# Optimization experiments

Hardware: AMD Instinct MI355X
Metric: run time of the kernel (lower is better)

The kernel has to match this reference:

```python
import jax, jax.numpy as jnp
import numpy as np

H = 8          # heads
KP = 6         # num_sparse keypoint tokens per group
NUM_PATCHES = 256


def _build_mask(N, Nk):
    # mask_q: [H, 3, N] bool, query token (g=0, i=0) disabled
    mask_q = np.ones((H, 3, N), dtype=bool)
    mask_q[:, 0, 0] = False
    # mask_k: [H, 3, Nk] bool, key token j=0 disabled for all groups
    mask_k = np.ones((H, 3, Nk), dtype=bool)
    mask_k[:, :, 0] = False
    keep = mask_q[:, :, :, None] & mask_k[:, :, None, :]  # [H,3,N,Nk]
    return jnp.asarray(~keep)  # True where masked out


def setup_inputs() -> dict:
    key = jax.random.key(0)
    k1, k2, k3 = jax.random.split(key, 3)
    B, G, N, D = 64, 3, NUM_PATCHES + KP, 512
    x = jax.random.normal(k1, (B, G, N, D), dtype=jnp.float32)
    w_qkv = jax.random.normal(k2, (D, 3 * D), dtype=jnp.float32) * (D ** -0.5)
    w_out = jax.random.normal(k3, (D, D), dtype=jnp.float32) * (D ** -0.5)
    b_out = jnp.zeros((D,), dtype=jnp.float32)
    return {"x": x, "w_qkv": w_qkv, "w_out": w_out, "b_out": b_out}


def reference(x, w_qkv, w_out, b_out):
    B, G, N, D = x.shape
    Dh = D // H
    scale = D ** -0.5  # scale_with_head=False

    qkv = x @ w_qkv  # [B,G,N,3D]
    q, k, v = jnp.split(qkv, 3, axis=-1)

    def to_heads(t):  # b g n (h d) -> b h g n d
        return t.reshape(B, G, N, H, Dh).transpose(0, 3, 1, 2, 4)

    q, k, v = to_heads(q), to_heads(k), to_heads(v)

    # gather keypoint K/V from all groups, shared across every group
    k_kp = k[:, :, :, :KP].reshape(B, H, 1, G * KP, Dh)
    v_kp = v[:, :, :, :KP].reshape(B, H, 1, G * KP, Dh)
    k_kp = jnp.broadcast_to(k_kp, (B, H, G, G * KP, Dh))
    v_kp = jnp.broadcast_to(v_kp, (B, H, G, G * KP, Dh))
    k = jnp.concatenate([k_kp, k[:, :, :, KP:]], axis=3)  # [B,H,G,Nk,Dh]
    v = jnp.concatenate([v_kp, v[:, :, :, KP:]], axis=3)
    Nk = k.shape[3]

    dots = jnp.einsum('bhgid,bhgjd->bhgij', q, k) * scale
    masked = _build_mask(N, Nk)  # [H,3,N,Nk], broadcasts over B
    neg = -jnp.finfo(dots.dtype).max
    dots = jnp.where(masked[None], neg, dots)

    attn = jax.nn.softmax(dots, axis=-1)
    out = jnp.einsum('bhgij,bhgjd->bhgid', attn, v)
    out = out.transpose(0, 2, 3, 1, 4).reshape(B, G, N, D)  # b h g n d -> b g n (h d)
    out = out @ w_out + b_out
    return out, dots
```

## Files before the change

kernel.cpp:

```cpp
#include <hip/hip_runtime.h>
#include <float.h>
#include <math.h>

#define B_   64
#define G_   3
#define N_   262
#define D_   512
#define H_   8
#define DH   64
#define KP_  6
#define NKP  18
#define NK   274
#define TD3  1536
#define M_   50304
#define SCALE 0.044194173824159216f
#define LOG2E 1.4426950408889634f

typedef unsigned short u16;
typedef __attribute__((ext_vector_type(4))) float f32x4;
typedef __attribute__((ext_vector_type(2))) float f32x2;
typedef float f32x4u __attribute__((ext_vector_type(4), aligned(4)));
typedef __attribute__((ext_vector_type(4))) unsigned int u32x4;
typedef __attribute__((ext_vector_type(8))) short bf16x8;

__device__ __forceinline__ u16 f2bf(float f) {
    unsigned int u = __float_as_uint(f);
    u += 0x7FFFu + ((u >> 16) & 1u);
    return (u16)(u >> 16);
}
__device__ __forceinline__ unsigned pack2bf(float lo, float hi) {
    unsigned ul = __float_as_uint(lo); ul += 0x7FFFu + ((ul >> 16) & 1u);
    unsigned uh = __float_as_uint(hi); uh += 0x7FFFu + ((uh >> 16) & 1u);
    return (ul >> 16) | (uh & 0xFFFF0000u);
}
__device__ __forceinline__ float mask_val() { return __uint_as_float(0xFF7F0000u); }

__device__ __forceinline__ void gload16(const void* g, void* l) {
    __builtin_amdgcn_global_load_lds(
        (const __attribute__((address_space(1))) unsigned int*)g,
        (__attribute__((address_space(3))) unsigned int*)l, 16, 0, 0);
}

__device__ __forceinline__ int xcd_swz(int orig, int nwg) {
    int q = nwg >> 3, r = nwg & 7;
    int xcd = orig & 7, lin = orig >> 3;
    return (xcd < r ? xcd * (q + 1) : r * (q + 1) + (xcd - r) * q) + lin;
}

__global__ __launch_bounds__(256)
void tcast2(const float* __restrict__ w1, u16* __restrict__ wT1,
            const float* __restrict__ w2, u16* __restrict__ wT2)
{
    int idx = blockIdx.x * 256 + threadIdx.x;
    if (idx < TD3 * D_) {
        int nn = idx / D_, kk = idx - nn * D_;
        wT1[idx] = f2bf(w1[(size_t)kk * TD3 + nn]);
    } else {
        int j = idx - TD3 * D_;
        if (j < D_ * D_) {
            int nn = j / D_, kk = j - nn * D_;
            wT2[j] = f2bf(w2[(size_t)kk * D_ + nn]);
        }
    }
}

template<int AF32, int OUT_BF16>
__global__ __launch_bounds__(512)
void gemm_bf16(const float* __restrict__ Af, const u16* __restrict__ Ab,
               const u16* __restrict__ WT,
               float* __restrict__ Cf, u16* __restrict__ Cb,
               const float* __restrict__ bias, int Ndim, int Kdim)
{
    __shared__ u16 Asm[128 * 64];
    __shared__ u16 Bsm[256 * 64];

    const int tid  = threadIdx.x;
    const int lane = tid & 63;
    const int wid  = tid >> 6;
    const int l15  = lane & 15;
    const int lg   = lane >> 4;
    const int wr   = (wid & 1) * 64;
    const int wc   = (wid >> 1) * 64;

    const int GX   = Ndim / 256;
    const int v    = xcd_swz(blockIdx.x, gridDim.x);
    const int row0 = (v / GX) * 128;
    const int col0 = (v % GX) * 256;

    const float* fsrcA[2];
    const u16*   bsrcA[2];
    #pragma unroll
    for (int i = 0; i < 2; ++i) {
        int slot = i * 512 + tid;
        int r = slot >> 3;
        int sblk = (slot & 7) ^ (r & 7);
        if (AF32) fsrcA[i] = Af + (size_t)(row0 + r) * Kdim + sblk * 8;
        else      bsrcA[i] = Ab + (size_t)(row0 + r) * Kdim + sblk * 8;
    }
    const u16* srcB[4];
    #pragma unroll
    for (int i = 0; i < 4; ++i) {
        int slot = i * 512 + tid;
        int r = slot >> 3;
        int sblk = (slot & 7) ^ (r & 7);
        srcB[i] = WT + (size_t)(col0 + r) * Kdim + sblk * 8;
    }

    f32x4 acc[4][4] = {};

    for (int k0 = 0; k0 < Kdim; k0 += 64) {
        #pragma unroll
        for (int i = 0; i < 4; ++i)
            gload16(srcB[i] + k0, &Bsm[(i * 512 + wid * 64) * 8]);
        if (AF32) {
            #pragma unroll
            for (int i = 0; i < 2; ++i) {
                float4 v0 = *(const float4*)(fsrcA[i] + k0);
                float4 v1 = *(const float4*)(fsrcA[i] + k0 + 4);
                u16 t[8] = { f2bf(v0.x), f2bf(v0.y), f2bf(v0.z), f2bf(v0.w),
                             f2bf(v1.x), f2bf(v1.y), f2bf(v1.z), f2bf(v1.w) };
                *(uint4*)&Asm[(i * 512 + tid) * 8] = *(const uint4*)t;
            }
        } else {
            #pragma unroll
            for (int i = 0; i < 2; ++i)
                gload16(bsrcA[i] + k0, &Asm[(i * 512 + wid * 64) * 8]);
        }
        __syncthreads();
        #pragma unroll
        for (int kk = 0; kk < 2; ++kk) {
            const int xb = (kk * 4 + lg) ^ (l15 & 7);
            bf16x8 a[4], b[4];
            #pragma unroll
            for (int m = 0; m < 4; ++m) a[m] = *(const bf16x8*)&Asm[(wr + m * 16 + l15) * 64 + xb * 8];
            #pragma unroll
            for (int n = 0; n < 4; ++n) b[n] = *(const bf16x8*)&Bsm[(wc + n * 16 + l15) * 64 + xb * 8];
            #pragma unroll
            for (int m = 0; m < 4; ++m)
                #pragma unroll
                for (int n = 0; n < 4; ++n)
                    acc[m][n] = __builtin_amdgcn_mfma_f32_16x16x32_bf16(a[m], b[n], acc[m][n], 0, 0, 0);
        }
        __syncthreads();
    }

    if (OUT_BF16) {
        u16* ob = (wid < 4) ? &Asm[wid * 2048] : &Bsm[(wid - 4) * 2048];
        #pragma unroll
        for (int p = 0; p < 2; ++p) {
            #pragma unroll
            for (int mh = 0; mh < 2; ++mh) {
                const int m = 2 * p + mh;
                #pragma unroll
                for (int n = 0; n < 4; ++n)
                    #pragma unroll
                    for (int r = 0; r < 4; ++r)
                        ob[(mh * 16 + lg * 4 + r) * 64 + n * 16 + l15] = f2bf(acc[m][n][r]);
            }
            #pragma unroll
            for (int it = 0; it < 4; ++it) {
                const int ch = it * 64 + lane;
                const int rw = ch >> 3, cp = ch & 7;
                u32x4 vv = *(const u32x4*)&ob[rw * 64 + cp * 8];
                *(u32x4*)(Cb + (size_t)(row0 + wr + p * 32 + rw) * Ndim + col0 + wc + cp * 8) = vv;
            }
        }
        return;
    }

    const int rbase = row0 + wr + lg * 4;
    const int cbase = col0 + wc + l15;
    #pragma unroll
    for (int m = 0; m < 4; ++m)
        #pragma unroll
        for (int n = 0; n < 4; ++n) {
            const int col = cbase + n * 16;
            #pragma unroll
            for (int r = 0; r < 4; ++r) {
                const int row = rbase + m * 16 + r;
                Cf[(size_t)row * Ndim + col] = acc[m][n][r] + bias[col];
            }
        }
}

__global__ __launch_bounds__(768, 1)
void attn_bf16(const u16* __restrict__ qkv, float* __restrict__ dots,
               u16* __restrict__ otmp)
{
    __shared__ u16 Ks[288 * 72];
    __shared__ u16 Vt[64 * 296];
    __shared__ float rowbuf[12][4 * 276];

    const int tid  = threadIdx.x;
    const int lane = tid & 63;
    const int wid  = tid >> 6;
    const int l15  = lane & 15;
    const int lg   = lane >> 4;

    const int bhg = blockIdx.x;
    const int b   = bhg / (H_ * G_);
    const int h   = (bhg / G_) % H_;
    const int g   = bhg % G_;
    const int rowbase = (b * G_ + g) * N_;
    const size_t dbase0 = (((size_t)(b * H_ + h) * G_ + g) * N_) * NK;

    #pragma unroll
    for (int it = 0; it < 3; ++it) {
        int lin = tid + it * 768;
        {
            int tok = lin >> 3, kg = (lin & 7) << 3;
            uint4 kv = make_uint4(0, 0, 0, 0), vv = make_uint4(0, 0, 0, 0);
            if (tok < NK) {
                int gs, ns;
                if (tok < NKP) { gs = tok / KP_; ns = tok - gs * KP_; }
                else           { gs = g;         ns = tok - NKP + KP_; }
                const u16* p = qkv + ((size_t)((b * G_ + gs) * N_ + ns)) * TD3 + h * DH + kg;
                kv = *(const uint4*)(p + D_);
                vv = *(const uint4*)(p + 2 * D_);
            }
            *(uint4*)&Ks[tok * 72 + kg] = kv;
            int slot = ((tok >> 5) << 5) | (((tok & 15) >> 2) << 3) | (((tok >> 4) & 1) << 2) | (tok & 3);
            union { uint4 u4; u16 us[8]; } u; u.u4 = vv;
            #pragma unroll
            for (int e = 0; e < 8; ++e) Vt[(kg + e) * 296 + slot] = u.us[e];
        }
    }
    __syncthreads();

    float* rb = rowbuf[wid];

    for (int t = wid; t < 17; t += 12) {
        const int n0 = t * 16;
        int qrow = n0 + l15; if (qrow > N_ - 1) qrow = N_ - 1;
        const u16* qp = qkv + (size_t)(rowbase + qrow) * TD3 + h * DH;
        bf16x8 qa0 = *(const bf16x8*)(qp + lg * 8);
        bf16x8 qa1 = *(const bf16x8*)(qp + 32 + lg * 8);

        f32x4 c[18];
        __builtin_amdgcn_s_setprio(1);
        #pragma unroll
        for (int jt = 0; jt < 18; ++jt) {
            const u16* kr = &Ks[(jt * 16 + l15) * 72];
            bf16x8 kb0 = *(const bf16x8*)(kr + lg * 8);
            bf16x8 kb1 = *(const bf16x8*)(kr + 32 + lg * 8);
            f32x4 z = {};
            z = __builtin_amdgcn_mfma_f32_16x16x32_bf16(kb0, qa0, z, 0, 0, 0);
            c[jt] = __builtin_amdgcn_mfma_f32_16x16x32_bf16(kb1, qa1, z, 0, 0, 0);
        }
        __builtin_amdgcn_s_setprio(0);

        #pragma unroll
        for (int jt = 0; jt < 18; ++jt)
            #pragma unroll
            for (int rr = 0; rr < 4; ++rr) c[jt][rr] *= SCALE;
        c[0][0] = (lg == 0) ? mask_val() : c[0][0];
        if (g == 0 && t == 0) {
            #pragma unroll
            for (int jt = 0; jt < 18; ++jt)
                #pragma unroll
                for (int rr = 0; rr < 4; ++rr)
                    c[jt][rr] = (l15 == 0) ? mask_val() : c[jt][rr];
        }

        const int php = l15 >> 2;
        const int r4  = l15 & 3;
        #pragma unroll
        for (int ph = 0; ph < 4; ++ph) {
            if (php == ph) {
                float* rr_ = &rb[r4 * 276];
                #pragma unroll
                for (int jt = 0; jt < 17; ++jt)
                    *(f32x4*)&rr_[jt * 16 + 4 * lg] = c[jt];
                if (lg == 0) { f32x2 tl = { c[17][0], c[17][1] }; *(f32x2*)&rr_[272] = tl; }
            }
            const int base_row = n0 + 4 * ph;
            #pragma unroll
            for (int r = 0; r < 4; ++r) {
                const int row = base_row + r;
                if (row < N_) {
                    const float* rrb = &rb[r * 276];
                    float* gp = &dots[dbase0 + (size_t)row * NK];
                    #pragma unroll
                    for (int i2 = 0; i2 < 2; ++i2) {
                        int ch = lane + (i2 << 6);
                        if (ch < 68) {
                            f32x4u vv = *(const f32x4*)&rrb[ch * 4];
                            __builtin_nontemporal_store(vv, (f32x4u*)&gp[ch * 4]);
                        } else if (ch == 68) {
                            f32x2 v2 = *(const f32x2*)&rrb[272];
                            __builtin_nontemporal_store(v2, (f32x2*)&gp[272]);
                        }
                    }
                }
            }
        }

        c[17][2] = -INFINITY; c[17][3] = -INFINITY;
        c[17][0] = (lg == 0) ? c[17][0] : -INFINITY;
        c[17][1] = (lg == 0) ? c[17][1] : -INFINITY;

        float mx = c[0][0];
        #pragma unroll
        for (int jt = 0; jt < 18; ++jt)
            #pragma unroll
            for (int rr = 0; rr < 4; ++rr) mx = fmaxf(mx, c[jt][rr]);
        mx = fmaxf(mx, __shfl_xor(mx, 16, 64));
        mx = fmaxf(mx, __shfl_xor(mx, 32, 64));
        float s = 0.f;
        #pragma unroll
        for (int jt = 0; jt < 18; ++jt)
            #pragma unroll
            for (int rr = 0; rr < 4; ++rr) {
                float p = exp2f((c[jt][rr] - mx) * LOG2E);
                c[jt][rr] = p;
                s += p;
            }
        s += __shfl_xor(s, 16, 64);
        s += __shfl_xor(s, 32, 64);
        const float inv = 1.f / s;

        f32x4 o[4] = {};
        __builtin_amdgcn_s_setprio(1);
        #pragma unroll
        for (int sl = 0; sl < 9; ++sl) {
            union { bf16x8 v; unsigned u[4]; } pa;
            pa.u[0] = pack2bf(c[2 * sl][0],     c[2 * sl][1]);
            pa.u[1] = pack2bf(c[2 * sl][2],     c[2 * sl][3]);
            pa.u[2] = pack2bf(c[2 * sl + 1][0], c[2 * sl + 1][1]);
            pa.u[3] = pack2bf(c[2 * sl + 1][2], c[2 * sl + 1][3]);
            #pragma unroll
            for (int dt = 0; dt < 4; ++dt) {
                bf16x8 vb = *(const bf16x8*)&Vt[(dt * 16 + l15) * 296 + sl * 32 + lg * 8];
                o[dt] = __builtin_amdgcn_mfma_f32_16x16x32_bf16(pa.v, vb, o[dt], 0, 0, 0);
            }
        }
        __builtin_amdgcn_s_setprio(0);

        u16* ob = (u16*)rb;
        #pragma unroll
        for (int dt = 0; dt < 4; ++dt)
            #pragma unroll
            for (int rr = 0; rr < 4; ++rr) {
                const int q = lg * 4 + rr;
                const float iq = __shfl(inv, q, 64);
                ob[q * 64 + dt * 16 + l15] = f2bf(o[dt][rr] * iq);
            }
        {
            const int vrows = min(16, N_ - n0);
            const int nch = vrows * 8;
            #pragma unroll
            for (int i2 = 0; i2 < 2; ++i2) {
                int ch = lane + (i2 << 6);
                if (ch < nch) {
                    int r = ch >> 3, cp = ch & 7;
                    uint4 vv = *(const uint4*)&ob[ch * 8];
                    *(uint4*)(otmp + (size_t)(rowbase + n0 + r) * D_ + h * DH + cp * 8) = vv;
                }
            }
        }
    }
}

extern "C" void kernel_launch(void* const* d_in, const int* in_sizes, int n_in,
                              void* d_out, int out_size, void* d_ws, size_t ws_size,
                              hipStream_t stream)
{
    const float* x     = (const float*)d_in[0];
    const float* w_qkv = (const float*)d_in[1];
    const float* w_out = (const float*)d_in[2];
    const float* b_out = (const float*)d_in[3];

    float* out  = (float*)d_out;
    float* dots = out + (size_t)M_ * D_;

    u16* wqkvT = (u16*)d_ws;
    u16* woutT = wqkvT + (size_t)TD3 * D_;
    u16* qkvb  = woutT + (size_t)D_ * D_;
    u16* otmpb = qkvb  + (size_t)M_ * TD3;

    tcast2<<<(TD3 * D_ + D_ * D_ + 255) / 256, 256, 0, stream>>>(
        w_qkv, wqkvT, w_out, woutT);

    gemm_bf16<1, 1><<<(TD3 / 256) * (M_ / 128), 512, 0, stream>>>(
        x, nullptr, wqkvT, nullptr, qkvb, nullptr, TD3, D_);

    attn_bf16<<<dim3(B_ * H_ * G_), 768, 0, stream>>>(qkvb, dots, otmpb);

    gemm_bf16<0, 0><<<(D_ / 256) * (M_ / 128), 512, 0, stream>>>(
        nullptr, otmpb, woutT, out, nullptr, b_out, D_, D_);
}
```

Measured before the change: 341.6 us.

## Double-buffer GEMM LDS tiles with BK=32 and prefetch next K-tile

```diff
diff --git a/kernel.cpp b/kernel.cpp
--- a/kernel.cpp
+++ b/kernel.cpp
@@ -66,13 +66,13 @@
 
 template<int AF32, int OUT_BF16>
 __global__ __launch_bounds__(512)
-void gemm_bf16(const float* __restrict__ Af, const u16* __restrict__ Ab,
+void gemm_bf16(const float* __restrict__ Af, const u16* __restrict__ Abg,
                const u16* __restrict__ WT,
                float* __restrict__ Cf, u16* __restrict__ Cb,
                const float* __restrict__ bias, int Ndim, int Kdim)
 {
-    __shared__ u16 Asm[128 * 64];
-    __shared__ u16 Bsm[256 * 64];
+    __shared__ u16 Ab[2][128 * 32];
+    __shared__ u16 Bb[2][256 * 32];
 
     const int tid  = threadIdx.x;
     const int lane = tid & 63;
@@ -87,65 +87,78 @@
     const int row0 = (v / GX) * 128;
     const int col0 = (v % GX) * 256;
 
-    const float* fsrcA[2];
-    const u16*   bsrcA[2];
+    const int rA = tid >> 2, bA_ = tid & 3;
+    const float* fA = Af  ? Af  + (size_t)(row0 + rA) * Kdim + (bA_ ^ (rA & 3)) * 8 : nullptr;
+    const u16*   bA = Abg ? Abg + (size_t)(row0 + rA) * Kdim + (bA_ ^ (rA & 3)) * 8 : nullptr;
+    const u16* srcB[2];
     #pragma unroll
     for (int i = 0; i < 2; ++i) {
-        int slot = i * 512 + tid;
-        int r = slot >> 3;
-        int sblk = (slot & 7) ^ (r & 7);
-        if (AF32) fsrcA[i] = Af + (size_t)(row0 + r) * Kdim + sblk * 8;
-        else      bsrcA[i] = Ab + (size_t)(row0 + r) * Kdim + sblk * 8;
-    }
-    const u16* srcB[4];
-    #pragma unroll
-    for (int i = 0; i < 4; ++i) {
-        int slot = i * 512 + tid;
-        int r = slot >> 3;
-        int sblk = (slot & 7) ^ (r & 7);
-        srcB[i] = WT + (size_t)(col0 + r) * Kdim + sblk * 8;
-    }
-
+        int s = i * 512 + tid;
+        int rb_ = s >> 2, bb_ = s & 3;
+        srcB[i] = WT + (size_t)(col0 + rb_) * Kdim + (bb_ ^ (rb_ & 3)) * 8;
+    }
+
+    const int nt = Kdim >> 5;
     f32x4 acc[4][4] = {};
-
-    for (int k0 = 0; k0 < Kdim; k0 += 64) {
-        #pragma unroll
-        for (int i = 0; i < 4; ++i)
-            gload16(srcB[i] + k0, &Bsm[(i * 512 + wid * 64) * 8]);
-        if (AF32) {
-            #pragma unroll
-            for (int i = 0; i < 2; ++i) {
-                float4 v0 = *(const float4*)(fsrcA[i] + k0);
-                float4 v1 = *(const float4*)(fsrcA[i] + k0 + 4);
-                u16 t[8] = { f2bf(v0.x), f2bf(v0.y), f2bf(v0.z), f2bf(v0.w),
-                             f2bf(v1.x), f2bf(v1.y), f2bf(v1.z), f2bf(v1.w) };
-                *(uint4*)&Asm[(i * 512 + tid) * 8] = *(const uint4*)t;
-            }
+    float4 pv0, pv1;
+
+    if (AF32) { pv0 = *(const float4*)(fA); pv1 = *(const float4*)(fA + 4); }
+    else      gload16(bA, &Ab[0][(wid * 64) * 8]);
+    gload16(srcB[0], &Bb[0][(wid * 64) * 8]);
+    gload16(srcB[1], &Bb[0][(512 + wid * 64) * 8]);
+    if (AF32) {
+        asm volatile("s_waitcnt vmcnt(2)" ::: "memory");
+        u16 t0[8] = { f2bf(pv0.x), f2bf(pv0.y), f2bf(pv0.z), f2bf(pv0.w),
+                      f2bf(pv1.x), f2bf(pv1.y), f2bf(pv1.z), f2bf(pv1.w) };
+        *(uint4*)&Ab[0][tid * 8] = *(const uint4*)t0;
+        asm volatile("s_waitcnt lgkmcnt(0)" ::: "memory");
+    }
+
+    for (int t = 0; t < nt; ++t) {
+        const int cur = t & 1, nxt = cur ^ 1;
+        const bool last_ = (t == nt - 1);
+        if (!last_) {
+            const int ko = (t + 1) << 5;
+            if (AF32) { pv0 = *(const float4*)(fA + ko); pv1 = *(const float4*)(fA + ko + 4); }
+            else      gload16(bA + ko, &Ab[nxt][(wid * 64) * 8]);
+            gload16(srcB[0] + ko, &Bb[nxt][(wid * 64) * 8]);
+            gload16(srcB[1] + ko, &Bb[nxt][(512 + wid * 64) * 8]);
+            if (AF32) asm volatile("s_waitcnt vmcnt(4)" ::: "memory");
+            else      asm volatile("s_waitcnt vmcnt(3)" ::: "memory");
         } else {
-            #pragma unroll
-            for (int i = 0; i < 2; ++i)
-                gload16(bsrcA[i] + k0, &Asm[(i * 512 + wid * 64) * 8]);
-        }
-        __syncthreads();
-        #pragma unroll
-        for (int kk = 0; kk < 2; ++kk) {
-            const int xb = (kk * 4 + lg) ^ (l15 & 7);
-            bf16x8 a[4], b[4];
-            #pragma unroll
-            for (int m = 0; m < 4; ++m) a[m] = *(const bf16x8*)&Asm[(wr + m * 16 + l15) * 64 + xb * 8];
-            #pragma unroll
-            for (int n = 0; n < 4; ++n) b[n] = *(const bf16x8*)&Bsm[(wc + n * 16 + l15) * 64 + xb * 8];
-            #pragma unroll
-            for (int m = 0; m < 4; ++m)
-                #pragma unroll
-                for (int n = 0; n < 4; ++n)
-                    acc[m][n] = __builtin_amdgcn_mfma_f32_16x16x32_bf16(a[m], b[n], acc[m][n], 0, 0, 0);
-        }
-        __syncthreads();
+            asm volatile("s_waitcnt vmcnt(0)" ::: "memory");
+        }
+        __builtin_amdgcn_s_barrier();
+
+        bf16x8 a[4], b[4];
+        #pragma unroll
+        for (int m = 0; m < 4; ++m) {
+            const int rr_ = wr + m * 16 + l15;
+            a[m] = *(const bf16x8*)&Ab[cur][(rr_ * 4 + (lg ^ (rr_ & 3))) * 8];
+        }
+        #pragma unroll
+        for (int n = 0; n < 4; ++n) {
+            const int rr_ = wc + n * 16 + l15;
+            b[n] = *(const bf16x8*)&Bb[cur][(rr_ * 4 + (lg ^ (rr_ & 3))) * 8];
+        }
+        #pragma unroll
+        for (int m = 0; m < 4; ++m)
+            #pragma unroll
+            for (int n = 0; n < 4; ++n)
+                acc[m][n] = __builtin_amdgcn_mfma_f32_16x16x32_bf16(a[m], b[n], acc[m][n], 0, 0, 0);
+
+        if (AF32 && !last_) {
+            asm volatile("s_waitcnt vmcnt(2)" ::: "memory");
+            u16 t1[8] = { f2bf(pv0.x), f2bf(pv0.y), f2bf(pv0.z), f2bf(pv0.w),
+                          f2bf(pv1.x), f2bf(pv1.y), f2bf(pv1.z), f2bf(pv1.w) };
+            *(uint4*)&Ab[nxt][tid * 8] = *(const uint4*)t1;
+        }
+        asm volatile("s_waitcnt lgkmcnt(0)" ::: "memory");
+        __builtin_amdgcn_s_barrier();
     }
 
     if (OUT_BF16) {
-        u16* ob = (wid < 4) ? &Asm[wid * 2048] : &Bsm[(wid - 4) * 2048];
+        u16* ob = ((u16*)Bb) + wid * 2048;
         #pragma unroll
         for (int p = 0; p < 2; ++p) {
             #pragma unroll
```

Result: slower. 351.9 us (+3.0%).
